# Optimization experiments

Hardware: AMD Instinct MI355X
Metric: run time of the kernel (lower is better)

## Reference

```python
import jax, jax.numpy as jnp
import numpy as np
import math

DIM = 3840
NUM_HEADS = 30
HEAD_DIM = 128
INNER = NUM_HEADS * HEAD_DIM
EPS = 1e-6


def rmsnorm(x, w):
    xf = x.astype(jnp.float32)
    var = jnp.mean(xf * xf, axis=-1, keepdims=True)
    return (w.astype(jnp.float32) * xf * jax.lax.rsqrt(var + EPS)).astype(x.dtype)


def setup_inputs() -> dict:
    key = jax.random.key(0)
    ks = jax.random.split(key, 10)
    s = 1.0 / math.sqrt(DIM)
    return {
        "x": jax.random.normal(ks[0], (2, 2048, DIM), dtype=jnp.float32),
        "Wq": jax.random.normal(ks[1], (DIM, INNER), dtype=jnp.float32) * s,
        "bq": jnp.zeros((INNER,), dtype=jnp.float32),
        "Wk": jax.random.normal(ks[2], (DIM, INNER), dtype=jnp.float32) * s,
        "bk": jnp.zeros((INNER,), dtype=jnp.float32),
        "Wv": jax.random.normal(ks[3], (DIM, INNER), dtype=jnp.float32) * s,
        "bv": jnp.zeros((INNER,), dtype=jnp.float32),
        "Wo": jax.random.normal(ks[4], (INNER, DIM), dtype=jnp.float32) * s,
        "bo": jnp.zeros((DIM,), dtype=jnp.float32),
        "gq": jnp.ones((INNER,), dtype=jnp.float32),
        "gk": jnp.ones((INNER,), dtype=jnp.float32),
    }


def reference(x, Wq, bq, Wk, bk, Wv, bv, Wo, bo, gq, gk):
    B, S, _ = x.shape
    q = rmsnorm(x @ Wq + bq, gq)  # [B,S,INNER]
    k = rmsnorm(x @ Wk + bk, gk)
    v = x @ Wv + bv
    # split heads: [B,H,S,D]
    q = q.reshape(B, S, NUM_HEADS, HEAD_DIM).transpose(0, 2, 1, 3)
    k = k.reshape(B, S, NUM_HEADS, HEAD_DIM).transpose(0, 2, 1, 3)
    v = v.reshape(B, S, NUM_HEADS, HEAD_DIM).transpose(0, 2, 1, 3)
    scale = 1.0 / math.sqrt(HEAD_DIM)
    attn = jnp.einsum("bhqd,bhkd->bhqk", q.astype(jnp.float32), k.astype(jnp.float32)) * scale
    attn = jax.nn.softmax(attn, axis=-1)
    out = jnp.einsum("bhqk,bhkd->bhqd", attn, v.astype(jnp.float32)).astype(q.dtype)
    out = out.transpose(0, 2, 1, 3).reshape(B, S, INNER)
    return out @ Wo + bo
```

## Files before the change

### kernel.cpp

```cpp
#include <hip/hip_runtime.h>


#define DIM 3840
#define NHEADS 30
#define HDIM 128
#define SEQ 2048
#define BATCH 2
#define MROWS (BATCH * SEQ)

typedef _Float16 h8 __attribute__((ext_vector_type(8)));
typedef _Float16 h4 __attribute__((ext_vector_type(4)));
typedef float f32x4 __attribute__((ext_vector_type(4)));

#define GP(p) ((const __attribute__((address_space(1))) void*)(p))
#define LP(p) ((__attribute__((address_space(3))) void*)(p))


__global__ __launch_bounds__(256) void convert_h_kernel(
    const float* __restrict__ in, _Float16* __restrict__ out, int n) {
  int i = (blockIdx.x * 256 + threadIdx.x) * 4;
  if (i + 3 < n) {
    float4 v = *reinterpret_cast<const float4*>(in + i);
    h4 o = {(_Float16)v.x, (_Float16)v.y, (_Float16)v.z, (_Float16)v.w};
    *reinterpret_cast<h4*>(out + i) = o;
  }
}

__global__ __launch_bounds__(256) void transpose_convert_kernel(
    const float* __restrict__ W, _Float16* __restrict__ Wt, int rows, int cols) {
  __shared__ float tile[32][33];
  int c0 = blockIdx.x * 32, r0 = blockIdx.y * 32;
  int tc = threadIdx.x & 31, tr = threadIdx.x >> 5;
#pragma unroll
  for (int i = 0; i < 32; i += 8)
    tile[tr + i][tc] = W[(size_t)(r0 + tr + i) * cols + c0 + tc];
  __syncthreads();
#pragma unroll
  for (int i = 0; i < 32; i += 8)
    Wt[(size_t)(c0 + tr + i) * rows + r0 + tc] = (_Float16)tile[tc][tr + i];
}

__global__ __launch_bounds__(256) void transpose_v_kernel(
    const _Float16* __restrict__ pre, _Float16* __restrict__ vT) {
  __shared__ _Float16 tile[32][33];
  int s0 = blockIdx.x * 32, d0 = blockIdx.y * 32, bh = blockIdx.z;
  int b = bh / NHEADS, h = bh % NHEADS;
  int tc = threadIdx.x & 31, tr = threadIdx.x >> 5;
#pragma unroll
  for (int i = 0; i < 32; i += 8) {
    int s = s0 + tr + i, d = d0 + tc;
    tile[tr + i][tc] = pre[((size_t)(b * SEQ + s)) * DIM + h * HDIM + d];
  }
  __syncthreads();
#pragma unroll
  for (int i = 0; i < 32; i += 8) {
    int d = d0 + tr + i, s = s0 + tc;
    vT[((size_t)bh * HDIM + d) * SEQ + s] = tile[tc][tr + i];
  }
}


template <typename OutT>
__global__ __launch_bounds__(512, 2) void gemm_bt_kernel(
    const _Float16* __restrict__ A, const _Float16* __restrict__ Bt,
    const float* __restrict__ bias, OutT* __restrict__ C,
    int M, int N, int K) {
  __shared__ __align__(16) _Float16 smem[65536];
  const int t = threadIdx.x;
  const int wave = t >> 6, lane = t & 63, quad = lane >> 4, l16 = lane & 15;

  const int nwg = gridDim.x;
  const int cpx = nwg >> 3;
  const int bid = blockIdx.x;
  const int swz = (bid & 7) * cpx + (bid >> 3);
  const int ntx = N >> 8;
  const int bm = (swz / ntx) << 8, bn = (swz % ntx) << 8;
  const int wm = (wave >> 2) * 128, wn = (wave & 3) * 64;

  const _Float16* Abase = A + (size_t)bm * K;
  const _Float16* Bbase = Bt + (size_t)bn * K;
  const int NT = K >> 6;

  f32x4 acc[8][4] = {};

  auto stage_half = [&](const _Float16* Gb, int d, int isB, int h, int k0) {
    _Float16* Lb = smem + d * 32768 + isB * 16384 + h * 8192;
#pragma unroll
    for (int L = 0; L < 2; ++L) {
      int slot = L * 512 + t;
      int row = h * 128 + (slot >> 3);
      int gs = (slot & 7) ^ (row & 7);
      __builtin_amdgcn_global_load_lds(GP(Gb + (size_t)row * K + k0 + gs * 8),
                                       LP(Lb + slot * 8), 16, 0, 0);
    }
  };

  stage_half(Bbase, 0, 1, 0, 0);  stage_half(Bbase, 0, 1, 1, 0);
  stage_half(Abase, 0, 0, 0, 0);  stage_half(Abase, 0, 0, 1, 0);
  stage_half(Bbase, 1, 1, 0, 64); stage_half(Bbase, 1, 1, 1, 64);
  asm volatile("s_waitcnt vmcnt(4)\n\ts_barrier" ::: "memory");

  for (int tt = 0; tt < NT; ++tt) {
    const _Float16* bufA = smem + (tt & 1) * 32768;
    const _Float16* bufB = bufA + 16384;
    const int dnx = (tt + 1) & 1;
    const int k1 = (tt + 1 < NT ? tt + 1 : NT - 1) << 6;
    const int k2 = (tt + 2 < NT ? tt + 2 : NT - 1) << 6;
    h8 afl[4], afh[4], bf[4];

#pragma unroll
    for (int ni = 0; ni < 4; ++ni) {
      int row = wn + ni * 16 + l16;
      bf[ni] = *reinterpret_cast<const h8*>(bufB + row * 64 + (quad ^ (row & 7)) * 8);
    }
#pragma unroll
    for (int mi = 0; mi < 4; ++mi) {
      int row = wm + mi * 16 + l16;
      afl[mi] = *reinterpret_cast<const h8*>(bufA + row * 64 + (quad ^ (row & 7)) * 8);
    }
    stage_half(Abase, dnx, 0, 0, k1);
    __builtin_amdgcn_s_barrier();
    asm volatile("s_waitcnt lgkmcnt(0)" ::: "memory");
    __builtin_amdgcn_sched_barrier(0);
    __builtin_amdgcn_s_setprio(1);
#pragma unroll
    for (int mi = 0; mi < 4; ++mi)
#pragma unroll
      for (int ni = 0; ni < 4; ++ni)
        acc[mi][ni] = __builtin_amdgcn_mfma_f32_16x16x32_f16(afl[mi], bf[ni], acc[mi][ni], 0, 0, 0);
    __builtin_amdgcn_s_setprio(0);
    __builtin_amdgcn_s_barrier();

#pragma unroll
    for (int mi = 0; mi < 4; ++mi) {
      int row = wm + 64 + mi * 16 + l16;
      afh[mi] = *reinterpret_cast<const h8*>(bufA + row * 64 + (quad ^ (row & 7)) * 8);
    }
    stage_half(Abase, dnx, 0, 1, k1);
    __builtin_amdgcn_s_barrier();
    asm volatile("s_waitcnt lgkmcnt(0)" ::: "memory");
    __builtin_amdgcn_sched_barrier(0);
    __builtin_amdgcn_s_setprio(1);
#pragma unroll
    for (int mi = 0; mi < 4; ++mi)
#pragma unroll
      for (int ni = 0; ni < 4; ++ni)
        acc[4 + mi][ni] = __builtin_amdgcn_mfma_f32_16x16x32_f16(afh[mi], bf[ni], acc[4 + mi][ni], 0, 0, 0);
    __builtin_amdgcn_s_setprio(0);
    __builtin_amdgcn_s_barrier();

#pragma unroll
    for (int ni = 0; ni < 4; ++ni) {
      int row = wn + ni * 16 + l16;
      bf[ni] = *reinterpret_cast<const h8*>(bufB + row * 64 + ((4 + quad) ^ (row & 7)) * 8);
    }
#pragma unroll
    for (int mi = 0; mi < 4; ++mi) {
      int row = wm + mi * 16 + l16;
      afl[mi] = *reinterpret_cast<const h8*>(bufA + row * 64 + ((4 + quad) ^ (row & 7)) * 8);
    }
    __builtin_amdgcn_s_barrier();
    asm volatile("s_waitcnt lgkmcnt(0)" ::: "memory");
    __builtin_amdgcn_sched_barrier(0);
    __builtin_amdgcn_s_setprio(1);
#pragma unroll
    for (int mi = 0; mi < 4; ++mi)
#pragma unroll
      for (int ni = 0; ni < 4; ++ni)
        acc[mi][ni] = __builtin_amdgcn_mfma_f32_16x16x32_f16(afl[mi], bf[ni], acc[mi][ni], 0, 0, 0);
    __builtin_amdgcn_s_setprio(0);
    __builtin_amdgcn_s_barrier();

#pragma unroll
    for (int mi = 0; mi < 4; ++mi) {
      int row = wm + 64 + mi * 16 + l16;
      afh[mi] = *reinterpret_cast<const h8*>(bufA + row * 64 + ((4 + quad) ^ (row & 7)) * 8);
    }
    stage_half(Bbase, tt & 1, 1, 0, k2);
    stage_half(Bbase, tt & 1, 1, 1, k2);
    __builtin_amdgcn_s_barrier();
    asm volatile("s_waitcnt lgkmcnt(0)" ::: "memory");
    __builtin_amdgcn_sched_barrier(0);
    __builtin_amdgcn_s_setprio(1);
#pragma unroll
    for (int mi = 0; mi < 4; ++mi)
#pragma unroll
      for (int ni = 0; ni < 4; ++ni)
        acc[4 + mi][ni] = __builtin_amdgcn_mfma_f32_16x16x32_f16(afh[mi], bf[ni], acc[4 + mi][ni], 0, 0, 0);
    __builtin_amdgcn_s_setprio(0);
    asm volatile("s_waitcnt vmcnt(4)\n\ts_barrier" ::: "memory");
  }

  asm volatile("s_waitcnt vmcnt(0)" ::: "memory");

#pragma unroll
  for (int ni = 0; ni < 4; ++ni) {
    int col = bn + wn + ni * 16 + l16;
    float bv = bias[col];
#pragma unroll
    for (int mi = 0; mi < 8; ++mi) {
      int row0 = bm + wm + mi * 16 + quad * 4;
#pragma unroll
      for (int r = 0; r < 4; ++r)
        C[(size_t)(row0 + r) * N + col] = (OutT)(acc[mi][ni][r] + bv);
    }
  }
}


__global__ __launch_bounds__(256) void rmsnorm_qk_kernel(
    const _Float16* __restrict__ pre, const float* __restrict__ g,
    _Float16* __restrict__ out, float extra_scale) {
  int row = blockIdx.x;
  const _Float16* p = pre + (size_t)row * DIM;
  float vals[15];
  float ss = 0.f;
#pragma unroll
  for (int it = 0; it < 15; ++it) {
    float v = (float)p[threadIdx.x + it * 256];
    vals[it] = v;
    ss += v * v;
  }
#pragma unroll
  for (int off = 32; off > 0; off >>= 1) ss += __shfl_down(ss, off, 64);
  __shared__ float red[4];
  if ((threadIdx.x & 63) == 0) red[threadIdx.x >> 6] = ss;
  __syncthreads();
  float scale = rsqrtf((red[0] + red[1] + red[2] + red[3]) * (1.f / DIM) + 1e-6f) * extra_scale;
  int b = row >> 11, s = row & (SEQ - 1);
#pragma unroll
  for (int it = 0; it < 15; ++it) {
    int i = threadIdx.x + it * 256;
    int h = i >> 7, d = i & 127;
    out[(((size_t)b * NHEADS + h) * SEQ + s) * HDIM + d] = (_Float16)(vals[it] * g[i] * scale);
  }
}


#define KOFF 0
#define VOFF 16384
#define POFF 32768

__global__ __launch_bounds__(256) void flash_attn_kernel(
    const _Float16* __restrict__ q, const _Float16* __restrict__ k,
    const _Float16* __restrict__ vT, _Float16* __restrict__ attnb) {
  __shared__ __align__(16) _Float16 smem[40960];
  const int t = threadIdx.x, wave = t >> 6, lane = t & 63, quad = lane >> 4, l16 = lane & 15;
  const int qt = blockIdx.x, bh = blockIdx.y, b = bh / NHEADS, h = bh % NHEADS;
  const _Float16* qbase = q + ((size_t)bh * SEQ + qt * 128) * HDIM;
  const _Float16* kbase = k + (size_t)bh * SEQ * HDIM;
  const _Float16* vbase = vT + (size_t)bh * HDIM * SEQ;
  const int wm = wave * 32;

#pragma unroll
  for (int j = 0; j < 8; ++j) {
    int row = j * 16 + (t >> 4);
    int c = (t & 15) ^ (row & 15);
    __builtin_amdgcn_global_load_lds(GP(qbase + (size_t)row * HDIM + c * 8),
                                     LP(smem + j * 2048 + wave * 512), 16, 0, 0);
  }
  __syncthreads();
  h8 qf[2][4];
#pragma unroll
  for (int mt = 0; mt < 2; ++mt)
#pragma unroll
    for (int ks = 0; ks < 4; ++ks) {
      int row = wm + mt * 16 + l16;
      qf[mt][ks] = *reinterpret_cast<const h8*>(
          smem + row * 128 + ((ks * 4 + quad) ^ (row & 15)) * 8);
    }
  __syncthreads();

  f32x4 oacc[2][8] = {};
  float lst[2][4] = {};

  auto stageKV = [&](int tile, int bufi) {
    const int kt = tile * 64;
    _Float16* kb_ = smem + KOFF + bufi * 8192;
    _Float16* vb_ = smem + VOFF + bufi * 8192;
#pragma unroll
    for (int j = 0; j < 4; ++j) {
      int row = j * 16 + (t >> 4);
      int c = (t & 15) ^ (row & 15);
      __builtin_amdgcn_global_load_lds(GP(kbase + (size_t)(kt + row) * HDIM + c * 8),
                                       LP(kb_ + j * 2048 + wave * 512), 16, 0, 0);
    }
#pragma unroll
    for (int j = 0; j < 4; ++j) {
      int row = j * 32 + (t >> 3);
      int c = (t & 7) ^ (row & 7);
      __builtin_amdgcn_global_load_lds(GP(vbase + (size_t)row * SEQ + kt + c * 8),
                                       LP(vb_ + j * 2048 + wave * 512), 16, 0, 0);
    }
  };

  stageKV(0, 0);
  stageKV(1, 1);

  for (int tt = 0; tt < SEQ / 64; ++tt) {
    asm volatile("s_waitcnt vmcnt(8)\n\ts_barrier" ::: "memory");

    const _Float16* kls = smem + KOFF + (tt & 1) * 8192;
    const _Float16* vls = smem + VOFF + (tt & 1) * 8192;

    f32x4 sacc[2][4] = {};
#pragma unroll
    for (int ks = 0; ks < 4; ++ks)
#pragma unroll
      for (int nt = 0; nt < 4; ++nt) {
        int rowB = nt * 16 + l16;
        h8 kf = *reinterpret_cast<const h8*>(
            kls + rowB * 128 + ((ks * 4 + quad) ^ (rowB & 15)) * 8);
#pragma unroll
        for (int mt = 0; mt < 2; ++mt)
          sacc[mt][nt] = __builtin_amdgcn_mfma_f32_16x16x32_f16(qf[mt][ks], kf, sacc[mt][nt], 0, 0, 0);
      }

#pragma unroll
    for (int mt = 0; mt < 2; ++mt)
#pragma unroll
      for (int nt = 0; nt < 4; ++nt) {
        int colg = nt * 2 + (l16 >> 3);
        int ce = l16 & 7;
#pragma unroll
        for (int r = 0; r < 4; ++r) {
          float e = __expf(sacc[mt][nt][r] - 12.0f);
          lst[mt][r] += e;
          int row = wm + mt * 16 + quad * 4 + r;
          smem[POFF + row * 64 + ((colg ^ (row & 7)) * 8) + ce] = (_Float16)e;
        }
      }

#pragma unroll
    for (int ks = 0; ks < 2; ++ks) {
      h8 pf[2];
#pragma unroll
      for (int mt = 0; mt < 2; ++mt) {
        int row = wm + mt * 16 + l16;
        pf[mt] = *reinterpret_cast<const h8*>(
            smem + POFF + row * 64 + ((ks * 4 + quad) ^ (row & 7)) * 8);
      }
#pragma unroll
      for (int nt = 0; nt < 8; ++nt) {
        int rowV = nt * 16 + l16;
        h8 vf = *reinterpret_cast<const h8*>(
            vls + rowV * 64 + ((ks * 4 + quad) ^ (rowV & 7)) * 8);
#pragma unroll
        for (int mt = 0; mt < 2; ++mt)
          oacc[mt][nt] = __builtin_amdgcn_mfma_f32_16x16x32_f16(pf[mt], vf, oacc[mt][nt], 0, 0, 0);
      }
    }

    asm volatile("s_barrier" ::: "memory");
    int dt = tt + 2;
    if (dt >= SEQ / 64) dt = SEQ / 64 - 1;
    stageKV(dt, tt & 1);
  }
  asm volatile("s_waitcnt vmcnt(0)" ::: "memory");

#pragma unroll
  for (int mt = 0; mt < 2; ++mt)
#pragma unroll
    for (int r = 0; r < 4; ++r) {
      float s = lst[mt][r];
#pragma unroll
      for (int off = 1; off <= 8; off <<= 1) s += __shfl_xor(s, off, 64);
      float inv = 1.f / s;
      int srow = qt * 128 + wm + mt * 16 + quad * 4 + r;
#pragma unroll
      for (int nt = 0; nt < 8; ++nt) {
        int d = nt * 16 + l16;
        attnb[((size_t)(b * SEQ + srow)) * DIM + h * HDIM + d] = (_Float16)(oacc[mt][nt][r] * inv);
      }
    }
}


extern "C" void kernel_launch(void* const* d_in, const int* in_sizes, int n_in,
                              void* d_out, int out_size, void* d_ws, size_t ws_size,
                              hipStream_t stream) {
  const float* x  = (const float*)d_in[0];
  const float* Wq = (const float*)d_in[1];
  const float* bq = (const float*)d_in[2];
  const float* Wk = (const float*)d_in[3];
  const float* bk = (const float*)d_in[4];
  const float* Wv = (const float*)d_in[5];
  const float* bv = (const float*)d_in[6];
  const float* Wo = (const float*)d_in[7];
  const float* bo = (const float*)d_in[8];
  const float* gq = (const float*)d_in[9];
  const float* gk = (const float*)d_in[10];
  float* out = (float*)d_out;

  char* ws = (char*)d_ws;
  _Float16* xb    = (_Float16*)(ws);
  _Float16* WT    = (_Float16*)(ws +  31457280LL);
  _Float16* qb    = (_Float16*)(ws +  60948480LL);
  _Float16* kb    = (_Float16*)(ws +  92405760LL);
  _Float16* vT    = (_Float16*)(ws + 123863040LL);
  _Float16* pre16 = (_Float16*)(ws + 155320320LL);
  _Float16* attnb = pre16;

  convert_h_kernel<<<15360, 256, 0, stream>>>(x, xb, MROWS * DIM);
  dim3 tgrid(DIM / 32, DIM / 32);
  const int ggrid = (DIM / 256) * (MROWS / 256);

  transpose_convert_kernel<<<tgrid, 256, 0, stream>>>(Wq, WT, DIM, DIM);
  gemm_bt_kernel<_Float16><<<ggrid, 512, 0, stream>>>(xb, WT, bq, pre16, MROWS, DIM, DIM);
  rmsnorm_qk_kernel<<<MROWS, 256, 0, stream>>>(pre16, gq, qb, 0.08838834764831845f);
  transpose_convert_kernel<<<tgrid, 256, 0, stream>>>(Wk, WT, DIM, DIM);
  gemm_bt_kernel<_Float16><<<ggrid, 512, 0, stream>>>(xb, WT, bk, pre16, MROWS, DIM, DIM);
  rmsnorm_qk_kernel<<<MROWS, 256, 0, stream>>>(pre16, gk, kb, 1.0f);
  transpose_convert_kernel<<<tgrid, 256, 0, stream>>>(Wv, WT, DIM, DIM);
  gemm_bt_kernel<_Float16><<<ggrid, 512, 0, stream>>>(xb, WT, bv, pre16, MROWS, DIM, DIM);
  dim3 vgrid(SEQ / 32, HDIM / 32, BATCH * NHEADS);
  transpose_v_kernel<<<vgrid, 256, 0, stream>>>(pre16, vT);

  dim3 agrid(SEQ / 128, BATCH * NHEADS);
  flash_attn_kernel<<<agrid, 256, 0, stream>>>(qb, kb, vT, attnb);

  transpose_convert_kernel<<<tgrid, 256, 0, stream>>>(Wo, WT, DIM, DIM);
  gemm_bt_kernel<float><<<ggrid, 512, 0, stream>>>(attnb, WT, bo, out, MROWS, DIM, DIM);
}
```

Baseline: 981.6 us.

## Double flash-attention query tile to 256 rows per block with precomputed LDS offsets

Each attention block now handles 256 query rows (64 per wave) instead of 128, so every staged K/V tile is reused across twice as many queries. This halves global K/V traffic and per-tile barrier overhead. The score loop is restructured per key subtile to limit live accumulators, and the LDS addresses are precomputed as byte offsets. The cost is more registers (larger qf and oacc), a bigger LDS footprint, and half as many blocks (480), which may reduce occupancy and load balance across CUs.

```diff
diff --git a/kernel.cpp b/kernel.cpp
--- a/kernel.cpp
+++ b/kernel.cpp
@@ -111,12 +111,12 @@
 #pragma unroll
     for (int ni = 0; ni < 4; ++ni) {
       int row = wn + ni * 16 + l16;
-      bf[ni] = *reinterpret_cast<const h8*>(bufB + row * 64 + (quad ^ (row & 7)) * 8);
+      bf[ni] = *reinterpret_cast<const h8*>(bufB + row * 64 + ((quad ^ (row & 7)) * 8));
     }
 #pragma unroll
     for (int mi = 0; mi < 4; ++mi) {
       int row = wm + mi * 16 + l16;
-      afl[mi] = *reinterpret_cast<const h8*>(bufA + row * 64 + (quad ^ (row & 7)) * 8);
+      afl[mi] = *reinterpret_cast<const h8*>(bufA + row * 64 + ((quad ^ (row & 7)) * 8));
     }
     stage_half(Abase, dnx, 0, 0, k1);
     __builtin_amdgcn_s_barrier();
@@ -134,7 +134,7 @@
 #pragma unroll
     for (int mi = 0; mi < 4; ++mi) {
       int row = wm + 64 + mi * 16 + l16;
-      afh[mi] = *reinterpret_cast<const h8*>(bufA + row * 64 + (quad ^ (row & 7)) * 8);
+      afh[mi] = *reinterpret_cast<const h8*>(bufA + row * 64 + ((quad ^ (row & 7)) * 8));
     }
     stage_half(Abase, dnx, 0, 1, k1);
     __builtin_amdgcn_s_barrier();
@@ -152,12 +152,12 @@
 #pragma unroll
     for (int ni = 0; ni < 4; ++ni) {
       int row = wn + ni * 16 + l16;
-      bf[ni] = *reinterpret_cast<const h8*>(bufB + row * 64 + ((4 + quad) ^ (row & 7)) * 8);
+      bf[ni] = *reinterpret_cast<const h8*>(bufB + row * 64 + (((4 + quad) ^ (row & 7)) * 8));
     }
 #pragma unroll
     for (int mi = 0; mi < 4; ++mi) {
       int row = wm + mi * 16 + l16;
-      afl[mi] = *reinterpret_cast<const h8*>(bufA + row * 64 + ((4 + quad) ^ (row & 7)) * 8);
+      afl[mi] = *reinterpret_cast<const h8*>(bufA + row * 64 + (((4 + quad) ^ (row & 7)) * 8));
     }
     __builtin_amdgcn_s_barrier();
     asm volatile("s_waitcnt lgkmcnt(0)" ::: "memory");
@@ -174,7 +174,7 @@
 #pragma unroll
     for (int mi = 0; mi < 4; ++mi) {
       int row = wm + 64 + mi * 16 + l16;
-      afh[mi] = *reinterpret_cast<const h8*>(bufA + row * 64 + ((4 + quad) ^ (row & 7)) * 8);
+      afh[mi] = *reinterpret_cast<const h8*>(bufA + row * 64 + (((4 + quad) ^ (row & 7)) * 8));
     }
     stage_half(Bbase, tt & 1, 1, 0, k2);
     stage_half(Bbase, tt & 1, 1, 1, k2);
@@ -237,116 +237,113 @@
 }
 
 
-#define KOFF 0
-#define VOFF 16384
-#define POFF 32768
-
 __global__ __launch_bounds__(256) void flash_attn_kernel(
     const _Float16* __restrict__ q, const _Float16* __restrict__ k,
     const _Float16* __restrict__ vT, _Float16* __restrict__ attnb) {
-  __shared__ __align__(16) _Float16 smem[40960];
+  __shared__ __align__(16) _Float16 smem[49152];
   const int t = threadIdx.x, wave = t >> 6, lane = t & 63, quad = lane >> 4, l16 = lane & 15;
   const int qt = blockIdx.x, bh = blockIdx.y, b = bh / NHEADS, h = bh % NHEADS;
-  const _Float16* qbase = q + ((size_t)bh * SEQ + qt * 128) * HDIM;
+  const _Float16* qbase = q + ((size_t)bh * SEQ + qt * 256) * HDIM;
   const _Float16* kbase = k + (size_t)bh * SEQ * HDIM;
   const _Float16* vbase = vT + (size_t)bh * HDIM * SEQ;
-  const int wm = wave * 32;
-
-#pragma unroll
-  for (int j = 0; j < 8; ++j) {
+  const int wq = wave * 64;
+
+#pragma unroll
+  for (int j = 0; j < 16; ++j) {
     int row = j * 16 + (t >> 4);
     int c = (t & 15) ^ (row & 15);
     __builtin_amdgcn_global_load_lds(GP(qbase + (size_t)row * HDIM + c * 8),
-                                     LP(smem + j * 2048 + wave * 512), 16, 0, 0);
+                                     LP(smem + j * 2048 + t * 8), 16, 0, 0);
   }
   __syncthreads();
-  h8 qf[2][4];
-#pragma unroll
-  for (int mt = 0; mt < 2; ++mt)
+  h8 qf[4][4];
+#pragma unroll
+  for (int mt = 0; mt < 4; ++mt)
 #pragma unroll
     for (int ks = 0; ks < 4; ++ks) {
-      int row = wm + mt * 16 + l16;
+      int row = wq + mt * 16 + l16;
       qf[mt][ks] = *reinterpret_cast<const h8*>(
-          smem + row * 128 + ((ks * 4 + quad) ^ (row & 15)) * 8);
+          smem + row * 128 + (((ks * 4 + quad) ^ l16) * 8));
     }
   __syncthreads();
 
-  f32x4 oacc[2][8] = {};
-  float lst[2][4] = {};
+  f32x4 oacc[4][8] = {};
+  float lst[4][4] = {};
 
   auto stageKV = [&](int tile, int bufi) {
     const int kt = tile * 64;
-    _Float16* kb_ = smem + KOFF + bufi * 8192;
-    _Float16* vb_ = smem + VOFF + bufi * 8192;
+    _Float16* kb_ = smem + bufi * 8192;
+    _Float16* vb_ = smem + 16384 + bufi * 8192;
 #pragma unroll
     for (int j = 0; j < 4; ++j) {
       int row = j * 16 + (t >> 4);
       int c = (t & 15) ^ (row & 15);
       __builtin_amdgcn_global_load_lds(GP(kbase + (size_t)(kt + row) * HDIM + c * 8),
-                                       LP(kb_ + j * 2048 + wave * 512), 16, 0, 0);
+                                       LP(kb_ + j * 2048 + t * 8), 16, 0, 0);
     }
 #pragma unroll
     for (int j = 0; j < 4; ++j) {
       int row = j * 32 + (t >> 3);
       int c = (t & 7) ^ (row & 7);
       __builtin_amdgcn_global_load_lds(GP(vbase + (size_t)row * SEQ + kt + c * 8),
-                                       LP(vb_ + j * 2048 + wave * 512), 16, 0, 0);
+                                       LP(vb_ + j * 2048 + t * 8), 16, 0, 0);
     }
   };
 
   stageKV(0, 0);
   stageKV(1, 1);
 
+  int kOff[4], vOff[2], pOff[2];
+#pragma unroll
+  for (int ks = 0; ks < 4; ++ks)
+    kOff[ks] = l16 * 256 + (((ks * 4 + quad) ^ l16) * 16);
+#pragma unroll
+  for (int ks = 0; ks < 2; ++ks) {
+    vOff[ks] = 32768 + l16 * 128 + (((ks * 4 + quad) ^ (l16 & 7)) * 16);
+    pOff[ks] = 65536 + (wq + l16) * 128 + (((ks * 4 + quad) ^ (l16 & 7)) * 16);
+  }
+  const char* smem_c = (const char*)smem;
+  char* smem_w = (char*)smem;
+
   for (int tt = 0; tt < SEQ / 64; ++tt) {
     asm volatile("s_waitcnt vmcnt(8)\n\ts_barrier" ::: "memory");
 
-    const _Float16* kls = smem + KOFF + (tt & 1) * 8192;
-    const _Float16* vls = smem + VOFF + (tt & 1) * 8192;
-
-    f32x4 sacc[2][4] = {};
-#pragma unroll
-    for (int ks = 0; ks < 4; ++ks)
-#pragma unroll
-      for (int nt = 0; nt < 4; ++nt) {
-        int rowB = nt * 16 + l16;
-        h8 kf = *reinterpret_cast<const h8*>(
-            kls + rowB * 128 + ((ks * 4 + quad) ^ (rowB & 15)) * 8);
-#pragma unroll
-        for (int mt = 0; mt < 2; ++mt)
-          sacc[mt][nt] = __builtin_amdgcn_mfma_f32_16x16x32_f16(qf[mt][ks], kf, sacc[mt][nt], 0, 0, 0);
+    const int kb = (tt & 1) << 14;
+
+#pragma unroll
+    for (int nt = 0; nt < 4; ++nt) {
+      f32x4 sacc[4] = {};
+#pragma unroll
+      for (int ks = 0; ks < 4; ++ks) {
+        h8 kf = *reinterpret_cast<const h8*>(smem_c + (kOff[ks] + kb) + nt * 4096);
+#pragma unroll
+        for (int mt = 0; mt < 4; ++mt)
+          sacc[mt] = __builtin_amdgcn_mfma_f32_16x16x32_f16(qf[mt][ks], kf, sacc[mt], 0, 0, 0);
       }
-
-#pragma unroll
-    for (int mt = 0; mt < 2; ++mt)
-#pragma unroll
-      for (int nt = 0; nt < 4; ++nt) {
-        int colg = nt * 2 + (l16 >> 3);
-        int ce = l16 & 7;
+      int colg = nt * 2 + (l16 >> 3);
+      int ce = l16 & 7;
+#pragma unroll
+      for (int mt = 0; mt < 4; ++mt)
 #pragma unroll
         for (int r = 0; r < 4; ++r) {
-          float e = __expf(sacc[mt][nt][r] - 12.0f);
+          float e = __expf(sacc[mt][r] - 12.0f);
           lst[mt][r] += e;
-          int row = wm + mt * 16 + quad * 4 + r;
-          smem[POFF + row * 64 + ((colg ^ (row & 7)) * 8) + ce] = (_Float16)e;
+          int rowl = quad * 4 + r;
+          smem[32768 + (wq + mt * 16 + rowl) * 64 + ((colg ^ (rowl & 7)) * 8) + ce] = (_Float16)e;
         }
-      }
+    }
 
 #pragma unroll
     for (int ks = 0; ks < 2; ++ks) {
-      h8 pf[2];
-#pragma unroll
-      for (int mt = 0; mt < 2; ++mt) {
-        int row = wm + mt * 16 + l16;
-        pf[mt] = *reinterpret_cast<const h8*>(
-            smem + POFF + row * 64 + ((ks * 4 + quad) ^ (row & 7)) * 8);
-      }
+      h8 pf[4];
+#pragma unroll
+      for (int mt = 0; mt < 4; ++mt)
+        pf[mt] = *reinterpret_cast<const h8*>(smem_c + pOff[ks] + mt * 2048);
 #pragma unroll
       for (int nt = 0; nt < 8; ++nt) {
-        int rowV = nt * 16 + l16;
-        h8 vf = *reinterpret_cast<const h8*>(
-            vls + rowV * 64 + ((ks * 4 + quad) ^ (rowV & 7)) * 8);
-#pragma unroll
-        for (int mt = 0; mt < 2; ++mt)
+        h8 vf = *reinterpret_cast<const h8*>(smem_c + (vOff[ks] + kb) + nt * 2048);
+#pragma unroll
+        for (int mt = 0; mt < 4; ++mt)
           oacc[mt][nt] = __builtin_amdgcn_mfma_f32_16x16x32_f16(pf[mt], vf, oacc[mt][nt], 0, 0, 0);
       }
     }
@@ -359,14 +356,14 @@
   asm volatile("s_waitcnt vmcnt(0)" ::: "memory");
 
 #pragma unroll
-  for (int mt = 0; mt < 2; ++mt)
+  for (int mt = 0; mt < 4; ++mt)
 #pragma unroll
     for (int r = 0; r < 4; ++r) {
       float s = lst[mt][r];
 #pragma unroll
       for (int off = 1; off <= 8; off <<= 1) s += __shfl_xor(s, off, 64);
       float inv = 1.f / s;
-      int srow = qt * 128 + wm + mt * 16 + quad * 4 + r;
+      int srow = qt * 256 + wq + mt * 16 + quad * 4 + r;
 #pragma unroll
       for (int nt = 0; nt < 8; ++nt) {
         int d = nt * 16 + l16;
@@ -416,7 +413,7 @@
   dim3 vgrid(SEQ / 32, HDIM / 32, BATCH * NHEADS);
   transpose_v_kernel<<<vgrid, 256, 0, stream>>>(pre16, vT);
 
-  dim3 agrid(SEQ / 128, BATCH * NHEADS);
+  dim3 agrid(SEQ / 256, BATCH * NHEADS);
   flash_attn_kernel<<<agrid, 256, 0, stream>>>(qb, kb, vT, attnb);
 
   transpose_convert_kernel<<<tgrid, 256, 0, stream>>>(Wo, WT, DIM, DIM);
```

Measured after the change: 980.8 us. No clear change (-0.1%).
